# Kernel optimization log

Measured on AMD Instinct MI355X. Metric: run time of the kernel, lower is better.

The kernel has to match this reference:

```python
import jax, jax.numpy as jnp
import numpy as np

NUM_HEADS = 16
D_MODEL = 1024
BATCH = 8
SEQ = 1024


def setup_inputs() -> dict:
    key = jax.random.key(0)
    ks = jax.random.split(key, 8)
    inv = 1.0 / np.sqrt(D_MODEL)
    return {
        "query": jax.random.normal(ks[0], (BATCH, SEQ, D_MODEL), dtype=jnp.float32),
        "key": jax.random.normal(ks[1], (BATCH, SEQ, D_MODEL), dtype=jnp.float32),
        "value": jax.random.normal(ks[2], (BATCH, SEQ, D_MODEL), dtype=jnp.float32),
        "mask": jax.random.randint(ks[3], (BATCH, SEQ), 0, 2, dtype=jnp.int32),
        "Wq": jax.random.normal(ks[4], (D_MODEL, D_MODEL), dtype=jnp.float32) * inv,
        "bq": jax.random.normal(ks[5], (D_MODEL,), dtype=jnp.float32) * inv,
        "Wo": jax.random.normal(ks[6], (D_MODEL, D_MODEL), dtype=jnp.float32) * inv,
        "bo": jax.random.normal(ks[7], (D_MODEL,), dtype=jnp.float32) * inv,
    }


def reference(query, key, value, mask, Wq, bq, Wo, bo):
    b, s, d = query.shape
    H = NUM_HEADS
    dk = d // H
    # NOTE: the original torch module (faithfully reproduced) applies
    # query_project to query, key AND value; key/value projections are dead.
    def proj(x):
        return (x @ Wq.T + bq).reshape(b, s, H, dk).transpose(0, 2, 1, 3)  # (b,H,s,dk)

    q, k, v = proj(query), proj(key), proj(value)

    m = mask.astype(query.dtype)                       # (b,s)
    score_mask = (m[:, :, None] * m[:, None, :])[:, None]  # (b,1,s,s), broadcasts over heads

    scale = 1.0 / jnp.sqrt(jnp.asarray(dk, dtype=query.dtype))
    score = jnp.einsum("bhqd,bhkd->bhqk", q, k) * scale  # (b,H,s,s)
    score = jnp.where(score_mask == 0, jnp.asarray(-1e9, dtype=score.dtype), score)
    # softmax then post-softmax mask multiply (the non-standard double-masking)
    p_attn = jax.nn.softmax(score, axis=-1) * score_mask  # (b,H,s,s)

    x = jnp.einsum("bhqk,bhkd->bhqd", p_attn, v)  # (b,H,s,dk)
    x = x.transpose(0, 2, 1, 3).reshape(b, s, d)
    out = x @ Wo.T + bo
    return out, p_attn
```

## Files before the change

kernel.cpp:

```cpp
#include <hip/hip_runtime.h>
#include <cstddef>
#include <cstdint>

#define BATCH   8
#define SEQ     1024
#define DMODEL  1024
#define NHEADS  16
#define DKH     64

typedef __attribute__((ext_vector_type(8))) short bf16x8;
typedef __attribute__((ext_vector_type(4))) short s16x4;
typedef __attribute__((ext_vector_type(4))) float f32x4;

#define MFMA16(a,b,c) __builtin_amdgcn_mfma_f32_16x16x32_bf16(a,b,c,0,0,0)

__device__ __forceinline__ unsigned short f2bf(float f) {
    uint32_t u = __float_as_uint(f);
    u += 0x7fffu + ((u >> 16) & 1u);
    return (unsigned short)(u >> 16);
}
__device__ __forceinline__ float bf2f(unsigned short s) {
    return __uint_as_float(((uint32_t)s) << 16);
}

__device__ __forceinline__ void gload16(const void* g, void* l) {
    __builtin_amdgcn_global_load_lds(
        (const __attribute__((address_space(1))) void*)g,
        (__attribute__((address_space(3))) void*)l, 16, 0, 0);
}

__global__ void cvt_hi(const float* __restrict__ src, unsigned short* __restrict__ hi, int n4)
{
    const int i = blockIdx.x * blockDim.x + threadIdx.x;
    if (i >= n4) return;
    const f32x4 v = ((const f32x4*)src)[i];
    s16x4 h4;
    #pragma unroll
    for (int e = 0; e < 4; ++e) h4[e] = (short)f2bf(v[e]);
    ((s16x4*)hi)[i] = h4;
}

#define GBM 128
#define GBN 128
#define GBK 32

template<int OUTMODE>
__global__ __launch_bounds__(256, 2)
void gemm_mfma(const unsigned short* __restrict__ Ab,
               const unsigned short* __restrict__ Whi, const float* __restrict__ bias,
               unsigned short* __restrict__ Ohi, float* __restrict__ Of)
{
    __shared__ unsigned short sT[2][2][GBM * GBK];

    const int tid = threadIdx.x, lane = tid & 63, wid = tid >> 6;
    const int m0 = blockIdx.y * GBM, n0 = blockIdx.x * GBN;
    const int wm = (wid >> 1) * 64, wn = (wid & 1) * 64;
    const int lo = lane & 15, hi4 = lane >> 4;

    const int gs = (lane & 3) ^ ((lane >> 3) & 3);
    const size_t arow0 = (size_t)(m0 + wid * 32 + (lane >> 2));
    const size_t wrow0 = (size_t)(n0 + wid * 32 + (lane >> 2));
    const unsigned short* aSrc0 = &Ab[arow0 * DMODEL + gs * 8];
    const unsigned short* aSrc1 = &Ab[(arow0 + 16) * DMODEL + gs * 8];
    const unsigned short* wSrc0 = &Whi[wrow0 * DMODEL + gs * 8];
    const unsigned short* wSrc1 = &Whi[(wrow0 + 16) * DMODEL + gs * 8];

    f32x4 acc[4][4] = {};

    {
        unsigned short* dA = &sT[0][0][(wid * 2) * 512];
        unsigned short* dW = &sT[0][1][(wid * 2) * 512];
        gload16(aSrc0, dA);       gload16(aSrc1, dA + 512);
        gload16(wSrc0, dW);       gload16(wSrc1, dW + 512);
    }

    for (int kt = 0; kt < DMODEL / GBK; ++kt) {
        __syncthreads();
        if (kt + 1 < DMODEL / GBK) {
            const int kn = (kt + 1) * GBK;
            unsigned short* dA = &sT[(kt + 1) & 1][0][(wid * 2) * 512];
            unsigned short* dW = &sT[(kt + 1) & 1][1][(wid * 2) * 512];
            gload16(aSrc0 + kn, dA);   gload16(aSrc1 + kn, dA + 512);
            gload16(wSrc0 + kn, dW);   gload16(wSrc1 + kn, dW + 512);
        }
        const unsigned short* aB = &sT[kt & 1][0][0];
        const unsigned short* wB = &sT[kt & 1][1][0];
        const int swz = (hi4 ^ ((lo >> 1) & 3)) * 8;
        bf16x8 ah[4], bh_[4];
        #pragma unroll
        for (int m = 0; m < 4; ++m)
            ah[m] = *(const bf16x8*)&aB[(wm + m * 16 + lo) * GBK + swz];
        #pragma unroll
        for (int n = 0; n < 4; ++n)
            bh_[n] = *(const bf16x8*)&wB[(wn + n * 16 + lo) * GBK + swz];
        #pragma unroll
        for (int m = 0; m < 4; ++m)
            #pragma unroll
            for (int n = 0; n < 4; ++n)
                acc[m][n] = MFMA16(ah[m], bh_[n], acc[m][n]);
    }

    #pragma unroll
    for (int n = 0; n < 4; ++n) {
        const int col = n0 + wn + n * 16 + lo;
        const float bv = bias[col];
        #pragma unroll
        for (int m = 0; m < 4; ++m) {
            if (OUTMODE == 1) {
                const int row0 = m0 + wm + m * 16 + hi4 * 4;
                const int b = row0 >> 10, s0_ = row0 & 1023;
                const int h = col >> 6, di = col & 63;
                s16x4 o;
                #pragma unroll
                for (int j = 0; j < 4; ++j) o[j] = (short)f2bf(acc[m][n][j] + bv);
                *(s16x4*)&Ohi[(((size_t)(b * NHEADS + h)) * DKH + di) * SEQ + s0_] = o;
            } else {
                #pragma unroll
                for (int j = 0; j < 4; ++j) {
                    const int row = m0 + wm + m * 16 + hi4 * 4 + j;
                    const float f = acc[m][n][j] + bv;
                    if (OUTMODE == 0) {
                        const int b = row >> 10, s = row & 1023;
                        const int h = col >> 6, di = col & 63;
                        Ohi[(((size_t)(b * NHEADS + h)) * SEQ + s) * DKH + di] = f2bf(f);
                    } else {
                        Of[(size_t)row * DMODEL + col] = f;
                    }
                }
            }
        }
    }
}

#define ALD 72

__global__ __launch_bounds__(256, 3)
void attn_fused(const unsigned short* __restrict__ qhi, const unsigned short* __restrict__ khi,
                const unsigned short* __restrict__ vt, const int* __restrict__ mask,
                float* __restrict__ pattn, unsigned short* __restrict__ xb)
{
    __shared__ unsigned short sQh[64 * ALD];
    __shared__ unsigned short sKh[64 * ALD];
    __shared__ unsigned short sVt[64 * ALD];
    __shared__ int sM[SEQ];
    __shared__ float sP32[4][16 * 68];

    const int blk = blockIdx.x;
    const int slot = blk >> 3;
    const int bh = (blk & 7) * 16 + (slot & 15);
    const int qt = slot >> 4;
    const int b = bh >> 4, h = bh & 15;
    const int q0 = qt * 64;
    const int tid = threadIdx.x, lane = tid & 63, wid = tid >> 6;
    const int lo = lane & 15, hi = lane >> 4;

    *(int4*)&sM[tid * 4] = *(const int4*)&mask[b * SEQ + tid * 4];
    #pragma unroll
    for (int c = 0; c < 2; ++c) {
        const int id = tid * 2 + c, row = id >> 3, col = (id & 7) * 8;
        *(bf16x8*)&sQh[row * ALD + col] =
            *(const bf16x8*)&qhi[((size_t)bh * SEQ + q0 + row) * DKH + col];
    }
    __syncthreads();

    const int qrow = wid * 16 + lo;
    bf16x8 aqh[2];
    aqh[0] = *(const bf16x8*)&sQh[qrow * ALD + hi * 8];
    aqh[1] = *(const bf16x8*)&sQh[qrow * ALD + 32 + hi * 8];
    int mqr[4];
    #pragma unroll
    for (int j = 0; j < 4; ++j) mqr[j] = sM[q0 + wid * 16 + hi * 4 + j];

    const int srow = tid >> 2, scol = (tid & 3) * 16;
    const unsigned short* kbase = &khi[(size_t)bh * SEQ * DKH + (size_t)srow * DKH + scol];
    const unsigned short* vbase = &vt[(size_t)bh * DKH * SEQ + (size_t)srow * SEQ + scol];

    float l4[4] = {0.f, 0.f, 0.f, 0.f};
    bf16x8 kr0 = *(const bf16x8*)(kbase);
    bf16x8 kr1 = *(const bf16x8*)(kbase + 8);
    for (int kt = 0; kt < 16; ++kt) {
        __syncthreads();
        *(bf16x8*)&sKh[srow * ALD + scol] = kr0;
        *(bf16x8*)&sKh[srow * ALD + scol + 8] = kr1;
        __syncthreads();
        if (kt < 15) {
            kr0 = *(const bf16x8*)(kbase + (size_t)(kt + 1) * 64 * DKH);
            kr1 = *(const bf16x8*)(kbase + (size_t)(kt + 1) * 64 * DKH + 8);
        }
        f32x4 acc4[4] = {};
        #pragma unroll
        for (int ks = 0; ks < 2; ++ks)
            #pragma unroll
            for (int n = 0; n < 4; ++n)
                acc4[n] = MFMA16(aqh[ks],
                    *(const bf16x8*)&sKh[(n * 16 + lo) * ALD + ks * 32 + hi * 8], acc4[n]);
        #pragma unroll
        for (int n = 0; n < 4; ++n) {
            const int mkc = sM[kt * 64 + n * 16 + lo];
            #pragma unroll
            for (int j = 0; j < 4; ++j)
                l4[j] += (mqr[j] && mkc) ? __expf(acc4[n][j] * 0.125f) : 0.f;
        }
    }
    float rinv[4];
    #pragma unroll
    for (int j = 0; j < 4; ++j) {
        float s = l4[j];
        #pragma unroll
        for (int o = 1; o < 16; o <<= 1) s += __shfl_xor(s, o, 16);
        rinv[j] = (s > 0.f) ? (1.0f / s) : 0.f;
    }

    f32x4 oacc[4] = {};
    kr0 = *(const bf16x8*)(kbase);
    kr1 = *(const bf16x8*)(kbase + 8);
    bf16x8 vr0 = *(const bf16x8*)(vbase);
    bf16x8 vr1 = *(const bf16x8*)(vbase + 8);
    for (int kt = 0; kt < 16; ++kt) {
        __syncthreads();
        *(bf16x8*)&sKh[srow * ALD + scol] = kr0;
        *(bf16x8*)&sKh[srow * ALD + scol + 8] = kr1;
        *(bf16x8*)&sVt[srow * ALD + scol] = vr0;
        *(bf16x8*)&sVt[srow * ALD + scol + 8] = vr1;
        __syncthreads();
        if (kt < 15) {
            kr0 = *(const bf16x8*)(kbase + (size_t)(kt + 1) * 64 * DKH);
            kr1 = *(const bf16x8*)(kbase + (size_t)(kt + 1) * 64 * DKH + 8);
            vr0 = *(const bf16x8*)(vbase + (kt + 1) * 64);
            vr1 = *(const bf16x8*)(vbase + (kt + 1) * 64 + 8);
        }
        f32x4 acc4[4] = {};
        #pragma unroll
        for (int ks = 0; ks < 2; ++ks)
            #pragma unroll
            for (int n = 0; n < 4; ++n)
                acc4[n] = MFMA16(aqh[ks],
                    *(const bf16x8*)&sKh[(n * 16 + lo) * ALD + ks * 32 + hi * 8], acc4[n]);

        #pragma unroll
        for (int n = 0; n < 4; ++n) {
            const int mkc = sM[kt * 64 + n * 16 + lo];
            #pragma unroll
            for (int j = 0; j < 4; ++j) {
                const float p = (mqr[j] && mkc) ? __expf(acc4[n][j] * 0.125f) * rinv[j] : 0.f;
                sP32[wid][(hi * 4 + j) * 68 + n * 16 + lo] = p;
            }
        }
        asm volatile("s_waitcnt lgkmcnt(0)" ::: "memory");
        __builtin_amdgcn_sched_barrier(0);

        #pragma unroll
        for (int rr = 0; rr < 4; ++rr) {
            const int prow = rr * 4 + hi;
            const f32x4 pv = *(const f32x4*)&sP32[wid][prow * 68 + lo * 4];
            *(f32x4*)&pattn[((size_t)bh * SEQ + q0 + wid * 16 + prow) * SEQ + kt * 64 + lo * 4] = pv;
        }
        #pragma unroll
        for (int ks = 0; ks < 2; ++ks) {
            const float* pp = &sP32[wid][lo * 68 + ks * 32 + hi * 8];
            const f32x4 p0 = *(const f32x4*)pp;
            const f32x4 p1 = *(const f32x4*)(pp + 4);
            bf16x8 ap;
            #pragma unroll
            for (int e = 0; e < 4; ++e) { ap[e] = (short)f2bf(p0[e]); ap[4 + e] = (short)f2bf(p1[e]); }
            #pragma unroll
            for (int n = 0; n < 4; ++n)
                oacc[n] = MFMA16(ap,
                    *(const bf16x8*)&sVt[(n * 16 + lo) * ALD + ks * 32 + hi * 8], oacc[n]);
        }
    }

    #pragma unroll
    for (int n = 0; n < 4; ++n)
        #pragma unroll
        for (int j = 0; j < 4; ++j) {
            const int row = q0 + wid * 16 + hi * 4 + j;
            const int col = h * DKH + n * 16 + lo;
            xb[(size_t)(b * SEQ + row) * DMODEL + col] = f2bf(oacc[n][j]);
        }
}

extern "C" void kernel_launch(void* const* d_in, const int* in_sizes, int n_in,
                              void* d_out, int out_size, void* d_ws, size_t ws_size,
                              hipStream_t stream) {
    (void)in_sizes; (void)n_in; (void)out_size; (void)ws_size;

    const float* query = (const float*)d_in[0];
    const float* key   = (const float*)d_in[1];
    const float* value = (const float*)d_in[2];
    const int*   mask  = (const int*)d_in[3];
    const float* Wq    = (const float*)d_in[4];
    const float* bq    = (const float*)d_in[5];
    const float* Wo    = (const float*)d_in[6];
    const float* bo    = (const float*)d_in[7];

    float* out   = (float*)d_out;
    float* pattn = out + (size_t)BATCH * SEQ * DMODEL;

    const size_t NE = (size_t)BATCH * SEQ * DMODEL;
    const size_t WE = (size_t)DMODEL * DMODEL;
    char* w = (char*)d_ws;
    unsigned short* wqhi = (unsigned short*)w;  w += WE * 2;
    unsigned short* wohi = (unsigned short*)w;  w += WE * 2;
    unsigned short* qbf  = (unsigned short*)w;  w += NE * 2;
    unsigned short* kbf  = (unsigned short*)w;  w += NE * 2;
    unsigned short* vbf  = (unsigned short*)w;  w += NE * 2;
    unsigned short* qhi  = (unsigned short*)w;  w += NE * 2;
    unsigned short* khi  = (unsigned short*)w;  w += NE * 2;
    unsigned short* vt   = (unsigned short*)w;  w += NE * 2;
    unsigned short* xb   = (unsigned short*)w;  w += NE * 2;

    const int wn4 = (int)(WE / 4);
    const int in4 = (int)(NE / 4);
    cvt_hi<<<(wn4 + 255) / 256, 256, 0, stream>>>(Wq, wqhi, wn4);
    cvt_hi<<<(wn4 + 255) / 256, 256, 0, stream>>>(Wo, wohi, wn4);
    cvt_hi<<<(in4 + 255) / 256, 256, 0, stream>>>(query, qbf, in4);
    cvt_hi<<<(in4 + 255) / 256, 256, 0, stream>>>(key,   kbf, in4);
    cvt_hi<<<(in4 + 255) / 256, 256, 0, stream>>>(value, vbf, in4);

    const dim3 gblk(DMODEL / GBN, (BATCH * SEQ) / GBM);

    gemm_mfma<0><<<gblk, 256, 0, stream>>>(qbf, wqhi, bq, qhi, nullptr);
    gemm_mfma<0><<<gblk, 256, 0, stream>>>(kbf, wqhi, bq, khi, nullptr);
    gemm_mfma<1><<<gblk, 256, 0, stream>>>(vbf, wqhi, bq, vt,  nullptr);

    attn_fused<<<BATCH * NHEADS * (SEQ / 64), 256, 0, stream>>>(qhi, khi, vt, mask, pattn, xb);

    gemm_mfma<2><<<gblk, 256, 0, stream>>>(xb, wohi, bo, nullptr, out);
}
```

Before: 319.3 us.

## Batch conversions and QKV projections into single launches, widen attention blocks

Merges the five fp32-to-bf16 conversion kernels into one launch and the three Q/K/V projection GEMMs into one grid over a stacked input, with segment-dependent epilogues. This cuts launch count and lets the GEMMs fill the device together. The attention kernel moves to 512-thread blocks that handle 128 query rows each, so each staged K/V tile is reused by twice as many rows, and each thread now loads 8 instead of 16 elements. The larger blocks use more shared memory per block, which may lower occupancy.

```diff
diff --git a/kernel.cpp b/kernel.cpp
--- a/kernel.cpp
+++ b/kernel.cpp
@@ -7,6 +7,10 @@
 #define DMODEL  1024
 #define NHEADS  16
 #define DKH     64
+#define NE      (BATCH*SEQ*DMODEL)
+#define WE      (DMODEL*DMODEL)
+#define NE4     (NE/4)
+#define WE4     (WE/4)
 
 typedef __attribute__((ext_vector_type(8))) short bf16x8;
 typedef __attribute__((ext_vector_type(4))) short s16x4;
@@ -29,15 +33,29 @@
         (__attribute__((address_space(3))) void*)l, 16, 0, 0);
 }
 
-__global__ void cvt_hi(const float* __restrict__ src, unsigned short* __restrict__ hi, int n4)
+__global__ void cvt_all(const float* __restrict__ q, const float* __restrict__ k,
+                        const float* __restrict__ v, const float* __restrict__ wq,
+                        const float* __restrict__ wo,
+                        unsigned short* __restrict__ qkv, unsigned short* __restrict__ wqh,
+                        unsigned short* __restrict__ woh)
 {
     const int i = blockIdx.x * blockDim.x + threadIdx.x;
-    if (i >= n4) return;
-    const f32x4 v = ((const f32x4*)src)[i];
+    const float* src; unsigned short* dst; int j;
+    if (i < 3 * NE4) {
+        const int seg = i >> 21;
+        j = i & (NE4 - 1);
+        src = (seg == 0) ? q : ((seg == 1) ? k : v);
+        dst = qkv + (size_t)seg * NE;
+    } else {
+        const int i2 = i - 3 * NE4;
+        if (i2 < WE4) { j = i2; src = wq; dst = wqh; }
+        else          { j = i2 - WE4; src = wo; dst = woh; }
+    }
+    const f32x4 x = ((const f32x4*)src)[j];
     s16x4 h4;
     #pragma unroll
-    for (int e = 0; e < 4; ++e) h4[e] = (short)f2bf(v[e]);
-    ((s16x4*)hi)[i] = h4;
+    for (int e = 0; e < 4; ++e) h4[e] = (short)f2bf(x[e]);
+    ((s16x4*)dst)[j] = h4;
 }
 
 #define GBM 128
@@ -48,7 +66,8 @@
 __global__ __launch_bounds__(256, 2)
 void gemm_mfma(const unsigned short* __restrict__ Ab,
                const unsigned short* __restrict__ Whi, const float* __restrict__ bias,
-               unsigned short* __restrict__ Ohi, float* __restrict__ Of)
+               unsigned short* __restrict__ Ohi, unsigned short* __restrict__ Ovt,
+               float* __restrict__ Of)
 {
     __shared__ unsigned short sT[2][2][GBM * GBK];
 
@@ -100,29 +119,32 @@
                 acc[m][n] = MFMA16(ah[m], bh_[n], acc[m][n]);
     }
 
+    const int seg = m0 >> 13;
     #pragma unroll
     for (int n = 0; n < 4; ++n) {
         const int col = n0 + wn + n * 16 + lo;
         const float bv = bias[col];
         #pragma unroll
         for (int m = 0; m < 4; ++m) {
-            if (OUTMODE == 1) {
-                const int row0 = m0 + wm + m * 16 + hi4 * 4;
+            if (OUTMODE == 3 && seg == 2) {
+                const int row0 = (m0 + wm + m * 16 + hi4 * 4) & 8191;
                 const int b = row0 >> 10, s0_ = row0 & 1023;
                 const int h = col >> 6, di = col & 63;
                 s16x4 o;
                 #pragma unroll
                 for (int j = 0; j < 4; ++j) o[j] = (short)f2bf(acc[m][n][j] + bv);
-                *(s16x4*)&Ohi[(((size_t)(b * NHEADS + h)) * DKH + di) * SEQ + s0_] = o;
+                *(s16x4*)&Ovt[(((size_t)(b * NHEADS + h)) * DKH + di) * SEQ + s0_] = o;
             } else {
                 #pragma unroll
                 for (int j = 0; j < 4; ++j) {
                     const int row = m0 + wm + m * 16 + hi4 * 4 + j;
                     const float f = acc[m][n][j] + bv;
-                    if (OUTMODE == 0) {
-                        const int b = row >> 10, s = row & 1023;
+                    if (OUTMODE == 3) {
+                        const int rs = row & 8191;
+                        const int b = rs >> 10, s = rs & 1023;
                         const int h = col >> 6, di = col & 63;
-                        Ohi[(((size_t)(b * NHEADS + h)) * SEQ + s) * DKH + di] = f2bf(f);
+                        unsigned short* dst = Ohi + (size_t)seg * NE;
+                        dst[(((size_t)(b * NHEADS + h)) * SEQ + s) * DKH + di] = f2bf(f);
                     } else {
                         Of[(size_t)row * DMODEL + col] = f;
                     }
@@ -134,27 +156,27 @@
 
 #define ALD 72
 
-__global__ __launch_bounds__(256, 3)
+__global__ __launch_bounds__(512, 4)
 void attn_fused(const unsigned short* __restrict__ qhi, const unsigned short* __restrict__ khi,
                 const unsigned short* __restrict__ vt, const int* __restrict__ mask,
                 float* __restrict__ pattn, unsigned short* __restrict__ xb)
 {
-    __shared__ unsigned short sQh[64 * ALD];
+    __shared__ unsigned short sQh[128 * ALD];
     __shared__ unsigned short sKh[64 * ALD];
     __shared__ unsigned short sVt[64 * ALD];
     __shared__ int sM[SEQ];
-    __shared__ float sP32[4][16 * 68];
+    __shared__ float sP32[8][16 * 68];
 
     const int blk = blockIdx.x;
-    const int slot = blk >> 3;
-    const int bh = (blk & 7) * 16 + (slot & 15);
-    const int qt = slot >> 4;
+    const int idx = blk >> 3;
+    const int bh = (blk & 7) * 16 + (idx & 15);
+    const int qt = idx >> 4;
     const int b = bh >> 4, h = bh & 15;
-    const int q0 = qt * 64;
+    const int q0 = qt * 128;
     const int tid = threadIdx.x, lane = tid & 63, wid = tid >> 6;
     const int lo = lane & 15, hi = lane >> 4;
 
-    *(int4*)&sM[tid * 4] = *(const int4*)&mask[b * SEQ + tid * 4];
+    *(int2*)&sM[tid * 2] = *(const int2*)&mask[b * SEQ + tid * 2];
     #pragma unroll
     for (int c = 0; c < 2; ++c) {
         const int id = tid * 2 + c, row = id >> 3, col = (id & 7) * 8;
@@ -171,22 +193,17 @@
     #pragma unroll
     for (int j = 0; j < 4; ++j) mqr[j] = sM[q0 + wid * 16 + hi * 4 + j];
 
-    const int srow = tid >> 2, scol = (tid & 3) * 16;
+    const int srow = tid >> 3, scol = (tid & 7) * 8;
     const unsigned short* kbase = &khi[(size_t)bh * SEQ * DKH + (size_t)srow * DKH + scol];
     const unsigned short* vbase = &vt[(size_t)bh * DKH * SEQ + (size_t)srow * SEQ + scol];
 
     float l4[4] = {0.f, 0.f, 0.f, 0.f};
-    bf16x8 kr0 = *(const bf16x8*)(kbase);
-    bf16x8 kr1 = *(const bf16x8*)(kbase + 8);
+    bf16x8 kr = *(const bf16x8*)kbase;
     for (int kt = 0; kt < 16; ++kt) {
         __syncthreads();
-        *(bf16x8*)&sKh[srow * ALD + scol] = kr0;
-        *(bf16x8*)&sKh[srow * ALD + scol + 8] = kr1;
-        __syncthreads();
-        if (kt < 15) {
-            kr0 = *(const bf16x8*)(kbase + (size_t)(kt + 1) * 64 * DKH);
-            kr1 = *(const bf16x8*)(kbase + (size_t)(kt + 1) * 64 * DKH + 8);
-        }
+        *(bf16x8*)&sKh[srow * ALD + scol] = kr;
+        __syncthreads();
+        if (kt < 15) kr = *(const bf16x8*)(kbase + (size_t)(kt + 1) * 64 * DKH);
         f32x4 acc4[4] = {};
         #pragma unroll
         for (int ks = 0; ks < 2; ++ks)
@@ -212,22 +229,16 @@
     }
 
     f32x4 oacc[4] = {};
-    kr0 = *(const bf16x8*)(kbase);
-    kr1 = *(const bf16x8*)(kbase + 8);
-    bf16x8 vr0 = *(const bf16x8*)(vbase);
-    bf16x8 vr1 = *(const bf16x8*)(vbase + 8);
+    kr = *(const bf16x8*)kbase;
+    bf16x8 vr = *(const bf16x8*)vbase;
     for (int kt = 0; kt < 16; ++kt) {
         __syncthreads();
-        *(bf16x8*)&sKh[srow * ALD + scol] = kr0;
-        *(bf16x8*)&sKh[srow * ALD + scol + 8] = kr1;
-        *(bf16x8*)&sVt[srow * ALD + scol] = vr0;
-        *(bf16x8*)&sVt[srow * ALD + scol + 8] = vr1;
+        *(bf16x8*)&sKh[srow * ALD + scol] = kr;
+        *(bf16x8*)&sVt[srow * ALD + scol] = vr;
         __syncthreads();
         if (kt < 15) {
-            kr0 = *(const bf16x8*)(kbase + (size_t)(kt + 1) * 64 * DKH);
-            kr1 = *(const bf16x8*)(kbase + (size_t)(kt + 1) * 64 * DKH + 8);
-            vr0 = *(const bf16x8*)(vbase + (kt + 1) * 64);
-            vr1 = *(const bf16x8*)(vbase + (kt + 1) * 64 + 8);
+            kr = *(const bf16x8*)(kbase + (size_t)(kt + 1) * 64 * DKH);
+            vr = *(const bf16x8*)(vbase + (kt + 1) * 64);
         }
         f32x4 acc4[4] = {};
         #pragma unroll
@@ -295,36 +306,26 @@
     const float* bo    = (const float*)d_in[7];
 
     float* out   = (float*)d_out;
-    float* pattn = out + (size_t)BATCH * SEQ * DMODEL;
-
-    const size_t NE = (size_t)BATCH * SEQ * DMODEL;
-    const size_t WE = (size_t)DMODEL * DMODEL;
+    float* pattn = out + (size_t)NE;
+
     char* w = (char*)d_ws;
-    unsigned short* wqhi = (unsigned short*)w;  w += WE * 2;
-    unsigned short* wohi = (unsigned short*)w;  w += WE * 2;
-    unsigned short* qbf  = (unsigned short*)w;  w += NE * 2;
-    unsigned short* kbf  = (unsigned short*)w;  w += NE * 2;
-    unsigned short* vbf  = (unsigned short*)w;  w += NE * 2;
-    unsigned short* qhi  = (unsigned short*)w;  w += NE * 2;
-    unsigned short* khi  = (unsigned short*)w;  w += NE * 2;
-    unsigned short* vt   = (unsigned short*)w;  w += NE * 2;
-    unsigned short* xb   = (unsigned short*)w;  w += NE * 2;
-
-    const int wn4 = (int)(WE / 4);
-    const int in4 = (int)(NE / 4);
-    cvt_hi<<<(wn4 + 255) / 256, 256, 0, stream>>>(Wq, wqhi, wn4);
-    cvt_hi<<<(wn4 + 255) / 256, 256, 0, stream>>>(Wo, wohi, wn4);
-    cvt_hi<<<(in4 + 255) / 256, 256, 0, stream>>>(query, qbf, in4);
-    cvt_hi<<<(in4 + 255) / 256, 256, 0, stream>>>(key,   kbf, in4);
-    cvt_hi<<<(in4 + 255) / 256, 256, 0, stream>>>(value, vbf, in4);
-
-    const dim3 gblk(DMODEL / GBN, (BATCH * SEQ) / GBM);
-
-    gemm_mfma<0><<<gblk, 256, 0, stream>>>(qbf, wqhi, bq, qhi, nullptr);
-    gemm_mfma<0><<<gblk, 256, 0, stream>>>(kbf, wqhi, bq, khi, nullptr);
-    gemm_mfma<1><<<gblk, 256, 0, stream>>>(vbf, wqhi, bq, vt,  nullptr);
-
-    attn_fused<<<BATCH * NHEADS * (SEQ / 64), 256, 0, stream>>>(qhi, khi, vt, mask, pattn, xb);
-
-    gemm_mfma<2><<<gblk, 256, 0, stream>>>(xb, wohi, bo, nullptr, out);
-}
+    unsigned short* wqhi = (unsigned short*)w;  w += (size_t)WE * 2;
+    unsigned short* wohi = (unsigned short*)w;  w += (size_t)WE * 2;
+    unsigned short* qkv  = (unsigned short*)w;  w += (size_t)NE * 3 * 2;
+    unsigned short* qhi  = (unsigned short*)w;  w += (size_t)NE * 2;
+    unsigned short* khi  = (unsigned short*)w;  w += (size_t)NE * 2;
+    unsigned short* vt   = (unsigned short*)w;  w += (size_t)NE * 2;
+    unsigned short* xb   = (unsigned short*)w;  w += (size_t)NE * 2;
+    (void)khi;
+
+    cvt_all<<<(3 * NE4 + 2 * WE4) / 256, 256, 0, stream>>>(
+        query, key, value, Wq, Wo, qkv, wqhi, wohi);
+
+    gemm_mfma<3><<<dim3(DMODEL / GBN, 3 * (BATCH * SEQ) / GBM), 256, 0, stream>>>(
+        qkv, wqhi, bq, qhi, vt, nullptr);
+
+    attn_fused<<<BATCH * NHEADS * (SEQ / 128), 512, 0, stream>>>(qhi, khi, vt, mask, pattn, xb);
+
+    gemm_mfma<2><<<dim3(DMODEL / GBN, (BATCH * SEQ) / GBM), 256, 0, stream>>>(
+        xb, wohi, bo, nullptr, nullptr, out);
+}
```

New measurement: 310.7 us. 2.7% less time.
